# Performance work log

Hardware: AMD Instinct MI355X
Metric: run time of the kernel (lower is better)

The kernel has to match this reference:

```python
import jax, jax.numpy as jnp
import numpy as np
from jax import lax

B, T, E, D, CC, K, H = 64, 2000, 512, 1024, 32, 31, 128
PAD = (K - 1) // 2


def setup_inputs() -> dict:
    key = jax.random.key(0)
    ks = jax.random.split(key, 12)
    enc_output = jax.random.normal(ks[0], (B, T, E), dtype=jnp.float32)
    text_len = jax.random.randint(ks[1], (B,), 1, T + 1)
    dec_state = jax.random.normal(ks[2], (B, D), dtype=jnp.float32)
    prev_att_w = jax.random.uniform(ks[3], (B, T), dtype=jnp.float32)
    # learned parameters
    W_enc = jax.random.normal(ks[4], (E, H), dtype=jnp.float32) / np.sqrt(E)
    b_enc = jnp.zeros((H,), dtype=jnp.float32)
    W_dec = jax.random.normal(ks[5], (D, H), dtype=jnp.float32) / np.sqrt(D)
    W_att = jax.random.normal(ks[6], (CC, H), dtype=jnp.float32) / np.sqrt(CC)
    conv_w = jax.random.normal(ks[7], (CC, 1, K), dtype=jnp.float32) / np.sqrt(K)  # OIH
    W_out = jax.random.normal(ks[8], (H, 1), dtype=jnp.float32) / np.sqrt(H)
    b_out = jnp.zeros((1,), dtype=jnp.float32)
    return {
        'enc_output': enc_output, 'text_len': text_len, 'dec_state': dec_state,
        'prev_att_w': prev_att_w, 'W_enc': W_enc, 'b_enc': b_enc, 'W_dec': W_dec,
        'W_att': W_att, 'conv_w': conv_w, 'W_out': W_out, 'b_out': b_out,
    }


def reference(enc_output, text_len, dec_state, prev_att_w,
              W_enc, b_enc, W_dec, W_att, conv_w, W_out, b_out):
    # processed_memory = fc_enc(enc_output): (B,T,H)
    pm = jnp.einsum('bte,eh->bth', enc_output, W_enc) + b_enc
    # location conv: (B,1,T) -> (B,CC,T), same padding, no bias
    att_conv = lax.conv_general_dilated(
        prev_att_w[:, None, :], conv_w, window_strides=(1,),
        padding=[(PAD, PAD)], dimension_numbers=('NCH', 'OIH', 'NCH'))
    # fc_att on channel dim: (B,T,H)
    att_conv = jnp.einsum('bct,ch->bth', att_conv, W_att)
    # fc_dec(dec_state): (B,1,H)
    dec = (dec_state @ W_dec)[:, None, :]
    # energy: (B,T)
    energy = (jnp.tanh(att_conv + pm + dec) @ W_out)[..., 0] + b_out[0]
    att_w = jax.nn.softmax(energy, axis=1)  # (B,T)
    att_c = jnp.einsum('bte,bt->be', enc_output, att_w)  # (B,E)
    return att_c, att_w
```

## Files before the change

### kernel.cpp

```cpp
#include <hip/hip_runtime.h>
#include <hip/hip_fp16.h>

typedef _Float16 f16x8 __attribute__((ext_vector_type(8)));
typedef float f32x4 __attribute__((ext_vector_type(4)));


__device__ __forceinline__ unsigned short f2h(float f) {
  __half h = __float2half(f);
  return __builtin_bit_cast(unsigned short, h);
}

__device__ __forceinline__ f16x8 u4_to_f16x8(uint4 v) {
  return __builtin_bit_cast(f16x8, v);
}

__device__ __forceinline__ f16x8 cvt8(float4 u, float4 v) {
  uint4 w;
  w.x = ((unsigned)f2h(u.y) << 16) | f2h(u.x);
  w.y = ((unsigned)f2h(u.w) << 16) | f2h(u.z);
  w.z = ((unsigned)f2h(v.y) << 16) | f2h(v.x);
  w.w = ((unsigned)f2h(v.w) << 16) | f2h(v.z);
  return u4_to_f16x8(w);
}

__device__ __forceinline__ float fast_tanh(float x) {
  return 1.f - 2.f / (__expf(2.f * x) + 1.f);
}

__global__ __launch_bounds__(256) void prep_kernel(
    const float* __restrict__ dec_state, const float* __restrict__ W_dec,
    const float* __restrict__ b_enc, const float* __restrict__ conv_w,
    const float* __restrict__ W_att, const float* __restrict__ W_enc,
    float* __restrict__ decb, unsigned short* __restrict__ MTg,
    unsigned short* __restrict__ WTpack)
{
  const int blk = blockIdx.x, tid = threadIdx.x;
  if (blk < 32) {
    __shared__ float sd[2048];
    const int sub = tid >> 7, h = tid & 127;
    const int b = blk*2 + sub;
    for (int i = h; i < 1024; i += 128) sd[sub*1024 + i] = dec_state[b*1024 + i];
    __syncthreads();
    float acc = b_enc[h];
    #pragma unroll 8
    for (int d = 0; d < 1024; ++d) acc = fmaf(sd[sub*1024 + d], W_dec[d*128 + h], acc);
    decb[b*128 + h] = acc;
  } else if (blk < 96) {
    const int e0 = (blk - 32) * 8;
    #pragma unroll
    for (int jj = 0; jj < 4; ++jj) {
      int idx = tid + jj*256;
      int el = idx >> 7, hh = idx & 127;
      int e = e0 + el;
      int kc = e >> 6, ks = (e >> 5) & 1, lg = (e >> 3) & 3, j = e & 7;
      int nt = hh >> 4, lr = hh & 15;
      int dst = (((kc*2 + ks)*8 + nt)*64 + lg*16 + lr)*8 + j;
      WTpack[dst] = f2h(W_enc[e*128 + hh]);
    }
  } else {
    if (tid < 128) {
      const int h = tid;
      for (int k = 0; k < 31; ++k) {
        float a = 0.f;
        #pragma unroll
        for (int c = 0; c < 32; ++c) a = fmaf(conv_w[c*31 + k], W_att[c*128 + h], a);
        MTg[h*32 + k] = f2h(a);
      }
      MTg[h*32 + 31] = 0;
    }
  }
}

__global__ __launch_bounds__(256, 4) void energy_kernel(
    const float* __restrict__ enc, const float* __restrict__ prev,
    const unsigned short* __restrict__ WTpack, const unsigned short* __restrict__ MTg,
    const float* __restrict__ decb, const float* __restrict__ W_out,
    float* __restrict__ energy)
{
  __shared__ float sPrev[160];
  __shared__ float sDecb[128];
  __shared__ float sWout[128];

  const int b  = blockIdx.y;
  const int t0 = blockIdx.x * 128;
  const int tid = threadIdx.x;
  const int wave = tid >> 6, lane = tid & 63;
  const int lr = lane & 15, lg = lane >> 4;

  if (tid < 128) { sDecb[tid] = decb[b*128 + tid]; sWout[tid] = W_out[tid]; }
  if (tid < 160) {
    int tt = t0 + tid - 15;
    sPrev[tid] = (tt >= 0 && tt < 2000) ? prev[b*2000 + tt] : 0.f;
  }
  __syncthreads();

  const float* encB = enc + (size_t)b * (2000u*512u);
  int tg0 = t0 + wave*32 + lr;       if (tg0 > 1999) tg0 = 1999;
  int tg1 = t0 + wave*32 + 16 + lr;  if (tg1 > 1999) tg1 = 1999;
  const float* row0 = encB + (size_t)tg0*512 + lg*8;
  const float* row1 = encB + (size_t)tg1*512 + lg*8;
  const char* wp = (const char*)WTpack + lane*16;

  f32x4 acc0[8], acc1[8];
  #pragma unroll
  for (int i = 0; i < 8; ++i) { acc0[i] = (f32x4){0,0,0,0}; acc1[i] = (f32x4){0,0,0,0}; }

  #pragma unroll
  for (int kc = 0; kc < 8; ++kc) {
    float4 u00 = *reinterpret_cast<const float4*>(row0 + kc*64);
    float4 v00 = *reinterpret_cast<const float4*>(row0 + kc*64 + 4);
    float4 u01 = *reinterpret_cast<const float4*>(row0 + kc*64 + 32);
    float4 v01 = *reinterpret_cast<const float4*>(row0 + kc*64 + 36);
    float4 u10 = *reinterpret_cast<const float4*>(row1 + kc*64);
    float4 v10 = *reinterpret_cast<const float4*>(row1 + kc*64 + 4);
    float4 u11 = *reinterpret_cast<const float4*>(row1 + kc*64 + 32);
    float4 v11 = *reinterpret_cast<const float4*>(row1 + kc*64 + 36);
    f16x8 a00 = cvt8(u00, v00);
    f16x8 a01 = cvt8(u01, v01);
    f16x8 a10 = cvt8(u10, v10);
    f16x8 a11 = cvt8(u11, v11);
    #pragma unroll
    for (int nt = 0; nt < 8; ++nt) {
      uint4 rb = *reinterpret_cast<const uint4*>(wp + ((kc*2 + 0)*8 + nt)*1024);
      f16x8 bbv = u4_to_f16x8(rb);
      acc0[nt] = __builtin_amdgcn_mfma_f32_16x16x32_f16(a00, bbv, acc0[nt], 0, 0, 0);
      acc1[nt] = __builtin_amdgcn_mfma_f32_16x16x32_f16(a10, bbv, acc1[nt], 0, 0, 0);
    }
    #pragma unroll
    for (int nt = 0; nt < 8; ++nt) {
      uint4 rb = *reinterpret_cast<const uint4*>(wp + ((kc*2 + 1)*8 + nt)*1024);
      f16x8 bbv = u4_to_f16x8(rb);
      acc0[nt] = __builtin_amdgcn_mfma_f32_16x16x32_f16(a01, bbv, acc0[nt], 0, 0, 0);
      acc1[nt] = __builtin_amdgcn_mfma_f32_16x16x32_f16(a11, bbv, acc1[nt], 0, 0, 0);
    }
  }

  {
    f16x8 a2_0, a2_1;
    const int pb0 = wave*32 + lr + lg*8;
    #pragma unroll
    for (int j = 0; j < 8; ++j) {
      a2_0[j] = __builtin_bit_cast(_Float16, f2h(sPrev[pb0 + j]));
      a2_1[j] = __builtin_bit_cast(_Float16, f2h(sPrev[pb0 + 16 + j]));
    }
    const char* mb = (const char*)MTg + lr*64 + lg*16;
    #pragma unroll
    for (int nt = 0; nt < 8; ++nt) {
      uint4 mv = *reinterpret_cast<const uint4*>(mb + nt*1024);
      f16x8 bbv = u4_to_f16x8(mv);
      acc0[nt] = __builtin_amdgcn_mfma_f32_16x16x32_f16(a2_0, bbv, acc0[nt], 0, 0, 0);
      acc1[nt] = __builtin_amdgcn_mfma_f32_16x16x32_f16(a2_1, bbv, acc1[nt], 0, 0, 0);
    }
  }

  #pragma unroll
  for (int mt = 0; mt < 2; ++mt) {
    float es0 = 0.f, es1 = 0.f, es2 = 0.f, es3 = 0.f;
    #pragma unroll
    for (int nt = 0; nt < 8; ++nt) {
      f32x4 a = (mt == 0) ? acc0[nt] : acc1[nt];
      float dh = sDecb[nt*16 + lr];
      float wo = sWout[nt*16 + lr];
      es0 += fast_tanh(a[0] + dh) * wo;
      es1 += fast_tanh(a[1] + dh) * wo;
      es2 += fast_tanh(a[2] + dh) * wo;
      es3 += fast_tanh(a[3] + dh) * wo;
    }
    #pragma unroll
    for (int off = 1; off < 16; off <<= 1) {
      es0 += __shfl_xor(es0, off, 64);
      es1 += __shfl_xor(es1, off, 64);
      es2 += __shfl_xor(es2, off, 64);
      es3 += __shfl_xor(es3, off, 64);
    }
    if (lr == 0) {
      const int t = t0 + wave*32 + mt*16 + lg*4;
      float ev[4] = {es0, es1, es2, es3};
      #pragma unroll
      for (int r = 0; r < 4; ++r)
        if (t + r < 2000) energy[b*2000 + t + r] = ev[r];
    }
  }
}

__global__ __launch_bounds__(256) void softmax_kernel(
    const float* __restrict__ energy, float* __restrict__ attw)
{
  const int b = blockIdx.x, tid = threadIdx.x;
  __shared__ float red[4];
  __shared__ float red2[4];
  float m = -1e30f;
  for (int i = tid; i < 2000; i += 256) m = fmaxf(m, energy[b*2000 + i]);
  #pragma unroll
  for (int off = 1; off < 64; off <<= 1) m = fmaxf(m, __shfl_xor(m, off, 64));
  if ((tid & 63) == 0) red[tid >> 6] = m;
  __syncthreads();
  m = fmaxf(fmaxf(red[0], red[1]), fmaxf(red[2], red[3]));

  float s = 0.f;
  for (int i = tid; i < 2000; i += 256) {
    float p = __expf(energy[b*2000 + i] - m);
    attw[b*2000 + i] = p;
    s += p;
  }
  #pragma unroll
  for (int off = 1; off < 64; off <<= 1) s += __shfl_xor(s, off, 64);
  if ((tid & 63) == 0) red2[tid >> 6] = s;
  __syncthreads();
  s = red2[0] + red2[1] + red2[2] + red2[3];
  float inv = 1.f / s;
  for (int i = tid; i < 2000; i += 256) attw[b*2000 + i] *= inv;
}

__global__ __launch_bounds__(256) void attc_partial_kernel(
    const float* __restrict__ enc, const float* __restrict__ attw,
    float* __restrict__ part)
{
  const int b = blockIdx.y, ch = blockIdx.x, tid = threadIdx.x;
  const int p = tid >> 7;
  const int e4 = (tid & 127) * 4;
  const int tstart = ch * 125 + p, tend = ch * 125 + 125;
  const float* encB = enc + (size_t)b * (2000u*512u);
  float a0 = 0.f, a1 = 0.f, a2 = 0.f, a3 = 0.f;
  #pragma unroll 2
  for (int t = tstart; t < tend; t += 2) {
    float w = attw[b*2000 + t];
    float4 v = *reinterpret_cast<const float4*>(encB + (size_t)t*512 + e4);
    a0 = fmaf(v.x, w, a0);
    a1 = fmaf(v.y, w, a1);
    a2 = fmaf(v.z, w, a2);
    a3 = fmaf(v.w, w, a3);
  }
  float4 out = {a0, a1, a2, a3};
  *reinterpret_cast<float4*>(part + ((size_t)(b*32 + ch*2 + p))*512 + e4) = out;
}

__global__ __launch_bounds__(128) void attc_reduce_kernel(
    const float* __restrict__ part, float* __restrict__ out)
{
  const int b = blockIdx.x, e4 = threadIdx.x * 4;
  float4 s = {0.f, 0.f, 0.f, 0.f};
  #pragma unroll
  for (int c = 0; c < 32; ++c) {
    float4 v = *reinterpret_cast<const float4*>(part + ((size_t)(b*32 + c))*512 + e4);
    s.x += v.x; s.y += v.y; s.z += v.z; s.w += v.w;
  }
  *reinterpret_cast<float4*>(out + b*512 + e4) = s;
}

extern "C" void kernel_launch(void* const* d_in, const int* in_sizes, int n_in,
                              void* d_out, int out_size, void* d_ws, size_t ws_size,
                              hipStream_t stream) {
  (void)in_sizes; (void)n_in; (void)out_size; (void)ws_size;
  const float* enc       = (const float*)d_in[0];
  const float* dec_state = (const float*)d_in[2];
  const float* prev      = (const float*)d_in[3];
  const float* W_enc     = (const float*)d_in[4];
  const float* b_enc     = (const float*)d_in[5];
  const float* W_dec     = (const float*)d_in[6];
  const float* W_att     = (const float*)d_in[7];
  const float* conv_w    = (const float*)d_in[8];
  const float* W_out     = (const float*)d_in[9];

  char* ws = (char*)d_ws;
  float*          energy = (float*)(ws + 0);
  float*          decb   = (float*)(ws + 524288);
  unsigned short* MTg    = (unsigned short*)(ws + 557056);
  unsigned short* WTpack = (unsigned short*)(ws + 565248);
  float*          part   = (float*)(ws + 696320);

  float* attc = (float*)d_out;
  float* attw = (float*)d_out + 64*512;

  prep_kernel        <<<97, 256, 0, stream>>>(dec_state, W_dec, b_enc, conv_w, W_att, W_enc,
                                              decb, MTg, WTpack);
  energy_kernel      <<<dim3(16, 64), 256, 0, stream>>>(enc, prev, WTpack, MTg, decb, W_out, energy);
  softmax_kernel     <<<64, 256, 0, stream>>>(energy, attw);
  attc_partial_kernel<<<dim3(16, 64), 256, 0, stream>>>(enc, attw, part);
  attc_reduce_kernel <<<64, 128, 0, stream>>>(part, attc);
}
```

Before: 173.5 us.

## Stage enc tile through LDS as fp16 MFMA fragments with coalesced loads

The energy kernel now loads each 64-row enc tile with fully coalesced float4 reads by all threads. It converts the values to fp16 once and writes them into LDS in an XOR-swizzled MFMA fragment layout. Each wave then reads its A fragments from LDS and processes one 16-row tile instead of two. This replaces the strided per-lane global reads that the old kernel made straight into registers. The cost is 64 KB of LDS per block, a lower occupancy hint (2), twice as many blocks, and W_enc fragments re-read from global by twice as many waves.

```diff
diff --git a/kernel.cpp b/kernel.cpp
--- a/kernel.cpp
+++ b/kernel.cpp
@@ -12,15 +12,6 @@
 
 __device__ __forceinline__ f16x8 u4_to_f16x8(uint4 v) {
   return __builtin_bit_cast(f16x8, v);
-}
-
-__device__ __forceinline__ f16x8 cvt8(float4 u, float4 v) {
-  uint4 w;
-  w.x = ((unsigned)f2h(u.y) << 16) | f2h(u.x);
-  w.y = ((unsigned)f2h(u.w) << 16) | f2h(u.z);
-  w.z = ((unsigned)f2h(v.y) << 16) | f2h(v.x);
-  w.w = ((unsigned)f2h(v.w) << 16) | f2h(v.z);
-  return u4_to_f16x8(w);
 }
 
 __device__ __forceinline__ float fast_tanh(float x) {
@@ -71,100 +62,101 @@
   }
 }
 
-__global__ __launch_bounds__(256, 4) void energy_kernel(
+__global__ __launch_bounds__(256, 2) void energy_kernel(
     const float* __restrict__ enc, const float* __restrict__ prev,
     const unsigned short* __restrict__ WTpack, const unsigned short* __restrict__ MTg,
     const float* __restrict__ decb, const float* __restrict__ W_out,
     float* __restrict__ energy)
 {
-  __shared__ float sPrev[160];
+  __shared__ __align__(16) unsigned short sFrag[4*16*64*8];
+  __shared__ float sPrev[96];
   __shared__ float sDecb[128];
   __shared__ float sWout[128];
 
   const int b  = blockIdx.y;
-  const int t0 = blockIdx.x * 128;
+  const int t0 = blockIdx.x * 64;
   const int tid = threadIdx.x;
   const int wave = tid >> 6, lane = tid & 63;
   const int lr = lane & 15, lg = lane >> 4;
 
   if (tid < 128) { sDecb[tid] = decb[b*128 + tid]; sWout[tid] = W_out[tid]; }
-  if (tid < 160) {
+  if (tid < 96) {
     int tt = t0 + tid - 15;
     sPrev[tid] = (tt >= 0 && tt < 2000) ? prev[b*2000 + tt] : 0.f;
   }
+
+  const float* encB = enc + (size_t)b * (2000u*512u);
+
+  {
+    const int row_half = tid >> 7;
+    const int e  = (tid & 127) * 4;
+    const int fs = e >> 5;
+    const int lge = (e >> 3) & 3;
+    const int jh  = e & 7;
+    char* sB = (char*)sFrag;
+    #pragma unroll 8
+    for (int c = 0; c < 32; ++c) {
+      int row = 2*c + row_half;
+      int tg = t0 + row; if (tg > 1999) tg = 1999;
+      float4 v = *reinterpret_cast<const float4*>(encB + (size_t)tg*512 + e);
+      int slot = (lge*16 + (row & 15)) ^ fs;
+      char* dst = sB + (row >> 4)*16384 + fs*1024 + slot*16 + jh*2;
+      uint2 wv;
+      wv.x = ((unsigned)f2h(v.y) << 16) | f2h(v.x);
+      wv.y = ((unsigned)f2h(v.w) << 16) | f2h(v.z);
+      *reinterpret_cast<uint2*>(dst) = wv;
+    }
+  }
   __syncthreads();
 
-  const float* encB = enc + (size_t)b * (2000u*512u);
-  int tg0 = t0 + wave*32 + lr;       if (tg0 > 1999) tg0 = 1999;
-  int tg1 = t0 + wave*32 + 16 + lr;  if (tg1 > 1999) tg1 = 1999;
-  const float* row0 = encB + (size_t)tg0*512 + lg*8;
-  const float* row1 = encB + (size_t)tg1*512 + lg*8;
+  const char* fbase = (const char*)sFrag + wave*16384;
   const char* wp = (const char*)WTpack + lane*16;
 
-  f32x4 acc0[8], acc1[8];
-  #pragma unroll
-  for (int i = 0; i < 8; ++i) { acc0[i] = (f32x4){0,0,0,0}; acc1[i] = (f32x4){0,0,0,0}; }
+  f32x4 acc[8];
+  #pragma unroll
+  for (int i = 0; i < 8; ++i) acc[i] = (f32x4){0,0,0,0};
 
   #pragma unroll
   for (int kc = 0; kc < 8; ++kc) {
-    float4 u00 = *reinterpret_cast<const float4*>(row0 + kc*64);
-    float4 v00 = *reinterpret_cast<const float4*>(row0 + kc*64 + 4);
-    float4 u01 = *reinterpret_cast<const float4*>(row0 + kc*64 + 32);
-    float4 v01 = *reinterpret_cast<const float4*>(row0 + kc*64 + 36);
-    float4 u10 = *reinterpret_cast<const float4*>(row1 + kc*64);
-    float4 v10 = *reinterpret_cast<const float4*>(row1 + kc*64 + 4);
-    float4 u11 = *reinterpret_cast<const float4*>(row1 + kc*64 + 32);
-    float4 v11 = *reinterpret_cast<const float4*>(row1 + kc*64 + 36);
-    f16x8 a00 = cvt8(u00, v00);
-    f16x8 a01 = cvt8(u01, v01);
-    f16x8 a10 = cvt8(u10, v10);
-    f16x8 a11 = cvt8(u11, v11);
-    #pragma unroll
-    for (int nt = 0; nt < 8; ++nt) {
-      uint4 rb = *reinterpret_cast<const uint4*>(wp + ((kc*2 + 0)*8 + nt)*1024);
-      f16x8 bbv = u4_to_f16x8(rb);
-      acc0[nt] = __builtin_amdgcn_mfma_f32_16x16x32_f16(a00, bbv, acc0[nt], 0, 0, 0);
-      acc1[nt] = __builtin_amdgcn_mfma_f32_16x16x32_f16(a10, bbv, acc1[nt], 0, 0, 0);
-    }
-    #pragma unroll
-    for (int nt = 0; nt < 8; ++nt) {
-      uint4 rb = *reinterpret_cast<const uint4*>(wp + ((kc*2 + 1)*8 + nt)*1024);
-      f16x8 bbv = u4_to_f16x8(rb);
-      acc0[nt] = __builtin_amdgcn_mfma_f32_16x16x32_f16(a01, bbv, acc0[nt], 0, 0, 0);
-      acc1[nt] = __builtin_amdgcn_mfma_f32_16x16x32_f16(a11, bbv, acc1[nt], 0, 0, 0);
+    const int fs0 = kc*2, fs1 = kc*2 + 1;
+    f16x8 a0 = *reinterpret_cast<const f16x8*>(fbase + fs0*1024 + ((lane ^ fs0) & 63)*16);
+    f16x8 a1 = *reinterpret_cast<const f16x8*>(fbase + fs1*1024 + ((lane ^ fs1) & 63)*16);
+    #pragma unroll
+    for (int nt = 0; nt < 8; ++nt) {
+      uint4 rb = *reinterpret_cast<const uint4*>(wp + (fs0*8 + nt)*1024);
+      acc[nt] = __builtin_amdgcn_mfma_f32_16x16x32_f16(a0, u4_to_f16x8(rb), acc[nt], 0, 0, 0);
+    }
+    #pragma unroll
+    for (int nt = 0; nt < 8; ++nt) {
+      uint4 rb = *reinterpret_cast<const uint4*>(wp + (fs1*8 + nt)*1024);
+      acc[nt] = __builtin_amdgcn_mfma_f32_16x16x32_f16(a1, u4_to_f16x8(rb), acc[nt], 0, 0, 0);
     }
   }
 
   {
-    f16x8 a2_0, a2_1;
-    const int pb0 = wave*32 + lr + lg*8;
-    #pragma unroll
-    for (int j = 0; j < 8; ++j) {
-      a2_0[j] = __builtin_bit_cast(_Float16, f2h(sPrev[pb0 + j]));
-      a2_1[j] = __builtin_bit_cast(_Float16, f2h(sPrev[pb0 + 16 + j]));
-    }
+    f16x8 a2;
+    const int pb0 = wave*16 + lr + lg*8;
+    #pragma unroll
+    for (int j = 0; j < 8; ++j)
+      a2[j] = __builtin_bit_cast(_Float16, f2h(sPrev[pb0 + j]));
     const char* mb = (const char*)MTg + lr*64 + lg*16;
     #pragma unroll
     for (int nt = 0; nt < 8; ++nt) {
       uint4 mv = *reinterpret_cast<const uint4*>(mb + nt*1024);
-      f16x8 bbv = u4_to_f16x8(mv);
-      acc0[nt] = __builtin_amdgcn_mfma_f32_16x16x32_f16(a2_0, bbv, acc0[nt], 0, 0, 0);
-      acc1[nt] = __builtin_amdgcn_mfma_f32_16x16x32_f16(a2_1, bbv, acc1[nt], 0, 0, 0);
-    }
-  }
-
-  #pragma unroll
-  for (int mt = 0; mt < 2; ++mt) {
+      acc[nt] = __builtin_amdgcn_mfma_f32_16x16x32_f16(a2, u4_to_f16x8(mv), acc[nt], 0, 0, 0);
+    }
+  }
+
+  {
     float es0 = 0.f, es1 = 0.f, es2 = 0.f, es3 = 0.f;
     #pragma unroll
     for (int nt = 0; nt < 8; ++nt) {
-      f32x4 a = (mt == 0) ? acc0[nt] : acc1[nt];
       float dh = sDecb[nt*16 + lr];
       float wo = sWout[nt*16 + lr];
-      es0 += fast_tanh(a[0] + dh) * wo;
-      es1 += fast_tanh(a[1] + dh) * wo;
-      es2 += fast_tanh(a[2] + dh) * wo;
-      es3 += fast_tanh(a[3] + dh) * wo;
+      es0 += fast_tanh(acc[nt][0] + dh) * wo;
+      es1 += fast_tanh(acc[nt][1] + dh) * wo;
+      es2 += fast_tanh(acc[nt][2] + dh) * wo;
+      es3 += fast_tanh(acc[nt][3] + dh) * wo;
     }
     #pragma unroll
     for (int off = 1; off < 16; off <<= 1) {
@@ -174,7 +166,7 @@
       es3 += __shfl_xor(es3, off, 64);
     }
     if (lr == 0) {
-      const int t = t0 + wave*32 + mt*16 + lg*4;
+      const int t = t0 + wave*16 + lg*4;
       float ev[4] = {es0, es1, es2, es3};
       #pragma unroll
       for (int r = 0; r < 4; ++r)
@@ -274,7 +266,7 @@
 
   prep_kernel        <<<97, 256, 0, stream>>>(dec_state, W_dec, b_enc, conv_w, W_att, W_enc,
                                               decb, MTg, WTpack);
-  energy_kernel      <<<dim3(16, 64), 256, 0, stream>>>(enc, prev, WTpack, MTg, decb, W_out, energy);
+  energy_kernel      <<<dim3(32, 64), 256, 0, stream>>>(enc, prev, WTpack, MTg, decb, W_out, energy);
   softmax_kernel     <<<64, 256, 0, stream>>>(energy, attw);
   attc_partial_kernel<<<dim3(16, 64), 256, 0, stream>>>(enc, attw, part);
   attc_reduce_kernel <<<64, 128, 0, stream>>>(part, attc);
```

Result: slower. 180.9 us (+4.2%).
